# Kernel tuning notes

Measured on AMD Instinct MI355X. Metric: run time of the kernel, lower is better.

## Reference

```python
import jax, jax.numpy as jnp
import numpy as np

B_, T_, DIM, HID, OUT, TAG = 128, 256, 512, 1024, 512, 64

def hard_sigmoid(x):
    return jnp.clip(0.2 * x + 0.5, 0.0, 1.0)

def setup_inputs() -> dict:
    key = jax.random.key(0)
    ks = jax.random.split(key, 8)
    s = 0.02  # weight scale for numerical stability under softmax
    return {
        "x": jax.random.normal(ks[0], (B_, T_, DIM), jnp.float32),
        "x0": jnp.zeros((B_, OUT), jnp.float32),
        "s0": jnp.zeros((B_, HID), jnp.float32),
        "W": jax.random.normal(ks[1], (OUT, 3 * HID), jnp.float32) * s,
        "U": jax.random.normal(ks[2], (HID, 3 * HID), jnp.float32) * s,
        "b": jnp.zeros((3 * HID,), jnp.float32),
        "W_x": jax.random.normal(ks[3], (HID, OUT), jnp.float32) * s,
        "b_x": jnp.zeros((OUT,), jnp.float32),
        "V_r": jax.random.normal(ks[4], (DIM, HID), jnp.float32) * s,
        "V_z": jax.random.normal(ks[5], (DIM, HID), jnp.float32) * s,
        "V_s": jax.random.normal(ks[6], (DIM, HID), jnp.float32) * s,
        "W_y": jax.random.normal(ks[7], (OUT, TAG), jnp.float32) * s,
        "b_y": jnp.zeros((TAG,), jnp.float32),
    }

def reference(x, x0, s0, W, U, b, W_x, b_x, V_r, V_z, V_s, W_y, b_y):
    h = HID
    W_r, W_z, W_s = W[:, :h], W[:, h:2*h], W[:, 2*h:]
    U_r, U_z, U_s = U[:, :h], U[:, h:2*h], U[:, 2*h:]
    b_r, b_z, b_s = b[:h], b[h:2*h], b[2*h:]

    def step(carry, inp):
        x_tm1, s_tm1 = carry
        xr = x_tm1 @ W_r + b_r + inp @ V_r
        xz = x_tm1 @ W_z + b_z + inp @ V_z
        r = hard_sigmoid(xr + s_tm1 @ U_r)
        z = hard_sigmoid(xz + s_tm1 @ U_z)
        xs = x_tm1 @ W_s + b_s + inp @ V_s
        s1 = jnp.tanh(xs + (r * s_tm1) @ U_s)
        s_t = (1.0 - z) * s_tm1 + z * s1
        x_t = jax.nn.softmax(s_t @ W_x + b_x, axis=-1)
        t_t = jax.nn.softmax(x_t @ W_y + b_y, axis=-1)
        return (x_t, s_t), t_t

    xs_seq = jnp.swapaxes(x, 0, 1)  # [T, B, dim]
    (_, _), t_seq = jax.lax.scan(step, (x0, s0), xs_seq)
    return jnp.swapaxes(t_seq, 0, 1)  # [B, T, tag]
```

## Files before the change

kernel.cpp:

```cpp
#include <hip/hip_runtime.h>
#include <math.h>

#define B_    128
#define T_    256
#define DIM_  512
#define HID_  1024
#define OUT_  512
#define TAG_  64
#define K3_   3072

typedef float f32x4 __attribute__((ext_vector_type(4)));
typedef short bf16x8 __attribute__((ext_vector_type(8)));
typedef unsigned uint32x4 __attribute__((ext_vector_type(4)));

#define MFMA(a,b,c) __builtin_amdgcn_mfma_f32_16x16x32_bf16(a,b,c,0,0,0)
#define DRAINV do{ asm volatile("s_waitcnt vmcnt(0)" ::: "memory"); __builtin_amdgcn_sched_barrier(0); }while(0)

__device__ __forceinline__ unsigned short f2b(float f){
    unsigned int u = __float_as_uint(f);
    u = (u + 0x7fffu + ((u >> 16) & 1u)) >> 16;
    return (unsigned short)u;
}
__device__ __forceinline__ float hardsig(float x){
    return fminf(fmaxf(0.2f*x + 0.5f, 0.f), 1.f);
}
__device__ __forceinline__ uint32x4 ld16(const void* p){
    return *(const uint32x4*)p;
}
__device__ __forceinline__ uint32x4 pack8f(const float* p){
    float4 a = *(const float4*)p;
    float4 b = *(const float4*)(p + 4);
    uint32x4 r;
    r.x = ((unsigned)f2b(a.y) << 16) | f2b(a.x);
    r.y = ((unsigned)f2b(a.w) << 16) | f2b(a.z);
    r.z = ((unsigned)f2b(b.y) << 16) | f2b(b.x);
    r.w = ((unsigned)f2b(b.w) << 16) | f2b(b.z);
    return r;
}

__global__ __launch_bounds__(256) void k_tr(
    unsigned short* __restrict__ dst, int dstride,
    const float* __restrict__ src, int ld, int col_off)
{
    __shared__ float tile[32][33];
    const int kb = blockIdx.x * 32, nb = blockIdx.y * 32;
    const int tx = threadIdx.x & 31, ty = threadIdx.x >> 5;
    #pragma unroll
    for (int i = 0; i < 4; ++i){
        int kl = ty + i*8;
        tile[kl][tx] = src[(size_t)(kb + kl)*ld + col_off + nb + tx];
    }
    __syncthreads();
    #pragma unroll
    for (int i = 0; i < 4; ++i){
        int nl = ty + i*8;
        dst[(size_t)(nb + nl)*dstride + kb + tx] = f2b(tile[tx][nl]);
    }
}
__global__ __launch_bounds__(256) void k_cvtx(
    const float4* __restrict__ src, ushort4* __restrict__ dst, int n4)
{
    int i = blockIdx.x * 256 + threadIdx.x;
    if (i < n4){
        float4 v = src[i];
        ushort4 o;
        o.x = f2b(v.x); o.y = f2b(v.y); o.z = f2b(v.z); o.w = f2b(v.w);
        dst[i] = o;
    }
}
__global__ __launch_bounds__(256) void k_init(
    const float* __restrict__ x0, const float* __restrict__ s0,
    unsigned short* __restrict__ xbufB, float* __restrict__ s_f,
    unsigned short* __restrict__ s_b)
{
    int i = blockIdx.x * 256 + threadIdx.x;
    if (i < B_*OUT_) xbufB[i] = f2b(x0[i]);
    if (i < B_*HID_){ s_f[i] = s0[i]; s_b[i] = f2b(s0[i]); }
}

__global__ __launch_bounds__(512) void k_gA(
    const unsigned short* __restrict__ xb16, const float* __restrict__ xf, int use_xb,
    const unsigned short* __restrict__ Wcat, const float* __restrict__ bias,
    const unsigned short* __restrict__ xbufB, const unsigned short* __restrict__ s_bb,
    const float* __restrict__ spf,
    unsigned short* __restrict__ rs_bb, float* __restrict__ pre_z,
    float* __restrict__ pre_xs, int t)
{
    __shared__ __align__(16) char smem[131072];
    const int wg   = blockIdx.x;
    const int tid  = threadIdx.x;
    const int lane = tid & 63;
    const int wv   = tid >> 6;
    const int l15  = lane & 15;
    const int kch  = lane >> 4;
    const int mt   = wv >> 2;
    const int ns   = wv & 3;
    const int axor = l15 & 7;

    const int npA = wg % 24, mpA = wg / 24;
    const int m0A = mpA*32, cA = npA*128, nsegA = npA >> 3;

    if (nsegA < 2){
        #pragma unroll
        for (int j = 0; j < 16; ++j){
            const int c = tid + j*512, row = c >> 8, k16 = c & 255;
            const int gr = m0A + row;
            uint32x4 v;
            if (k16 < 64)       v = ld16(xbufB + gr*512 + k16*8);
            else if (k16 < 128){
                if (use_xb)     v = ld16(xb16 + ((size_t)gr*T_ + t)*DIM_ + (k16-64)*8);
                else            v = pack8f(xf + ((size_t)gr*T_ + t)*DIM_ + (k16-64)*8);
            } else              v = ld16(s_bb + gr*1024 + (k16-128)*8);
            *(uint32x4*)(smem + row*4096 + ((k16 ^ (row & 7)) << 4)) = v;
        }
    } else {
        #pragma unroll
        for (int j = 0; j < 8; ++j){
            const int c = tid + j*512, row = c >> 7, k16 = c & 127;
            const int gr = m0A + row;
            uint32x4 v;
            if (k16 < 64)       v = ld16(xbufB + gr*512 + k16*8);
            else {
                if (use_xb)     v = ld16(xb16 + ((size_t)gr*T_ + t)*DIM_ + (k16-64)*8);
                else            v = pack8f(xf + ((size_t)gr*T_ + t)*DIM_ + (k16-64)*8);
            }
            *(uint32x4*)(smem + row*4096 + ((k16 ^ (row & 7)) << 4)) = v;
        }
    }
    __syncthreads();

    const int c0 = cA + ns*32;
    const int kmax = (nsegA < 2) ? 2048 : 1024;
    const unsigned short* bp0 = Wcat + (size_t)(c0 + l15)*2048 + kch*8;
    const unsigned short* bp1 = bp0 + (size_t)16*2048;
    f32x4 acc0 = {0.f,0.f,0.f,0.f}, acc1 = {0.f,0.f,0.f,0.f};
    const int abase = (mt*16 + l15)*4096;
    #pragma unroll 8
    for (int kb = 0; kb < kmax; kb += 32){
        bf16x8 a = *(const bf16x8*)(smem + abase + ((((kb>>3)+kch) ^ axor) << 4));
        acc0 = MFMA(a, *(const bf16x8*)(bp0 + kb), acc0);
        acc1 = MFMA(a, *(const bf16x8*)(bp1 + kb), acc1);
    }
    const int rbA = m0A + mt*16 + kch*4;
    if (nsegA == 0){
        #pragma unroll
        for (int h = 0; h < 2; ++h){
            f32x4 acc = h ? acc1 : acc0;
            const int col = c0 + h*16 + l15;
            const float bv = bias[col];
            #pragma unroll
            for (int q = 0; q < 4; ++q){
                float rs = hardsig(acc[q] + bv) * spf[(size_t)(rbA+q)*1024 + col];
                rs_bb[(size_t)(rbA+q)*1024 + col] = f2b(rs);
            }
        }
    } else if (nsegA == 1){
        #pragma unroll
        for (int h = 0; h < 2; ++h){
            f32x4 acc = h ? acc1 : acc0;
            const int col = c0 + h*16 + l15;
            const float bv = bias[col];
            #pragma unroll
            for (int q = 0; q < 4; ++q)
                pre_z[(size_t)(rbA+q)*1024 + (col - 1024)] = acc[q] + bv;
        }
    } else {
        #pragma unroll
        for (int h = 0; h < 2; ++h){
            f32x4 acc = h ? acc1 : acc0;
            const int col = c0 + h*16 + l15;
            const float bv = bias[col];
            #pragma unroll
            for (int q = 0; q < 4; ++q)
                pre_xs[(size_t)(rbA+q)*1024 + (col - 2048)] = acc[q] + bv;
        }
    }
}

__global__ __launch_bounds__(512) void k_gB(
    const unsigned short* __restrict__ Ust,
    const unsigned short* __restrict__ rs_bb,
    const float* __restrict__ pre_z, const float* __restrict__ pre_xs,
    const float* __restrict__ spf,
    float* __restrict__ snf, unsigned short* __restrict__ s_bb)
{
    __shared__ __align__(16) char smem[65536];
    const int wg   = blockIdx.x;
    const int tid  = threadIdx.x;
    const int lane = tid & 63;
    const int wv   = tid >> 6;
    const int l15  = lane & 15;
    const int kch  = lane >> 4;
    const int mt   = wv >> 2;
    const int ns   = wv & 3;
    const int axor = l15 & 7;
    const int np = wg % 8, mp = wg / 8;
    const int m0B = mp*32, cB = np*128;

    #pragma unroll
    for (int j = 0; j < 8; ++j){
        const int c = tid + j*512, row = c >> 7, k16 = c & 127;
        uint32x4 v = ld16(rs_bb + (size_t)(m0B+row)*1024 + k16*8);
        *(uint32x4*)(smem + row*2048 + ((k16 ^ (row & 7)) << 4)) = v;
    }
    __syncthreads();

    const int c0 = cB + ns*32;
    const unsigned short* bp0 = Ust + (size_t)(c0 + l15)*1024 + kch*8;
    const unsigned short* bp1 = bp0 + (size_t)16*1024;
    f32x4 acc0 = {0.f,0.f,0.f,0.f}, acc1 = {0.f,0.f,0.f,0.f};
    const int abase = (mt*16 + l15)*2048;
    #pragma unroll 8
    for (int kb = 0; kb < 1024; kb += 32){
        bf16x8 a = *(const bf16x8*)(smem + abase + ((((kb>>3)+kch) ^ axor) << 4));
        acc0 = MFMA(a, *(const bf16x8*)(bp0 + kb), acc0);
        acc1 = MFMA(a, *(const bf16x8*)(bp1 + kb), acc1);
    }
    const int rbB = m0B + mt*16 + kch*4;
    #pragma unroll
    for (int h = 0; h < 2; ++h){
        f32x4 acc = h ? acc1 : acc0;
        const int col = c0 + h*16 + l15;
        #pragma unroll
        for (int q = 0; q < 4; ++q){
            const size_t idx = (size_t)(rbB+q)*1024 + col;
            float z  = hardsig(pre_z[idx]);
            float sv = (1.f - z)*spf[idx] + z*tanhf(pre_xs[idx] + acc[q]);
            snf[idx]  = sv;
            s_bb[idx] = f2b(sv);
        }
    }
}

__global__ __launch_bounds__(512) void k_gC(
    const unsigned short* __restrict__ Wxt,
    const unsigned short* __restrict__ s_bb,
    const float* __restrict__ bx, float* __restrict__ logits)
{
    __shared__ __align__(16) char smem[65536];
    const int wg   = blockIdx.x;
    const int tid  = threadIdx.x;
    const int lane = tid & 63;
    const int wv   = tid >> 6;
    const int l15  = lane & 15;
    const int kch  = lane >> 4;
    const int mt   = wv >> 2;
    const int ns   = wv & 3;
    const int axor = l15 & 7;
    const int np = wg % 4, mp = wg / 4;
    const int m0C = mp*32, cC = np*128;

    #pragma unroll
    for (int j = 0; j < 8; ++j){
        const int c = tid + j*512, row = c >> 7, k16 = c & 127;
        uint32x4 v = ld16(s_bb + (size_t)(m0C+row)*1024 + k16*8);
        *(uint32x4*)(smem + row*2048 + ((k16 ^ (row & 7)) << 4)) = v;
    }
    __syncthreads();

    const int c0 = cC + ns*32;
    const unsigned short* bp0 = Wxt + (size_t)(c0 + l15)*1024 + kch*8;
    const unsigned short* bp1 = bp0 + (size_t)16*1024;
    f32x4 acc0 = {0.f,0.f,0.f,0.f}, acc1 = {0.f,0.f,0.f,0.f};
    const int abase = (mt*16 + l15)*2048;
    #pragma unroll 8
    for (int kb = 0; kb < 1024; kb += 32){
        bf16x8 a = *(const bf16x8*)(smem + abase + ((((kb>>3)+kch) ^ axor) << 4));
        acc0 = MFMA(a, *(const bf16x8*)(bp0 + kb), acc0);
        acc1 = MFMA(a, *(const bf16x8*)(bp1 + kb), acc1);
    }
    const int rbC = m0C + mt*16 + kch*4;
    #pragma unroll
    for (int h = 0; h < 2; ++h){
        f32x4 acc = h ? acc1 : acc0;
        const int col = c0 + h*16 + l15;
        const float bv = bx[col];
        #pragma unroll
        for (int q = 0; q < 4; ++q)
            logits[(size_t)(rbC+q)*512 + col] = acc[q] + bv;
    }
}

__global__ __launch_bounds__(256) void k_soft(
    const float* __restrict__ logits, const float* __restrict__ Wy,
    const float* __restrict__ by, unsigned short* __restrict__ xbufB,
    float* __restrict__ out, int t)
{
    __shared__ float xs[512];
    __shared__ float red[256];
    const int r = blockIdx.x, tid = threadIdx.x;
    float v0 = logits[r*OUT_ + tid];
    float v1 = logits[r*OUT_ + 256 + tid];
    red[tid] = fmaxf(v0, v1);
    __syncthreads();
    for (int s = 128; s > 0; s >>= 1){
        if (tid < s) red[tid] = fmaxf(red[tid], red[tid+s]);
        __syncthreads();
    }
    float mx = red[0];
    __syncthreads();
    float e0 = expf(v0 - mx), e1 = expf(v1 - mx);
    red[tid] = e0 + e1;
    __syncthreads();
    for (int s = 128; s > 0; s >>= 1){
        if (tid < s) red[tid] += red[tid+s];
        __syncthreads();
    }
    float inv = 1.f / red[0];
    __syncthreads();
    float x0v = e0*inv, x1v = e1*inv;
    xs[tid] = x0v; xs[tid + 256] = x1v;
    xbufB[r*OUT_ + tid] = f2b(x0v);
    xbufB[r*OUT_ + 256 + tid] = f2b(x1v);
    __syncthreads();
    const int j = tid & 63, part = tid >> 6;
    float p = 0.f;
    const int k0 = part * 128;
    #pragma unroll 4
    for (int k = k0; k < k0 + 128; ++k) p += xs[k] * Wy[k*TAG_ + j];
    red[tid] = p;
    __syncthreads();
    if (tid < 64){
        float tl = red[tid] + red[tid+64] + red[tid+128] + red[tid+192] + by[tid];
        float wm = tl;
        #pragma unroll
        for (int off = 32; off > 0; off >>= 1) wm = fmaxf(wm, __shfl_xor(wm, off));
        float ex = expf(tl - wm);
        float sm = ex;
        #pragma unroll
        for (int off = 32; off > 0; off >>= 1) sm += __shfl_xor(sm, off);
        out[((long)r*T_ + t)*TAG_ + tid] = ex / sm;
    }
}

extern "C" void kernel_launch(void* const* d_in, const int* in_sizes, int n_in,
                              void* d_out, int out_size, void* d_ws, size_t ws_size,
                              hipStream_t stream){
    const float* x   = (const float*)d_in[0];
    const float* x0  = (const float*)d_in[1];
    const float* s0  = (const float*)d_in[2];
    const float* W   = (const float*)d_in[3];
    const float* U   = (const float*)d_in[4];
    const float* b   = (const float*)d_in[5];
    const float* Wx  = (const float*)d_in[6];
    const float* bx  = (const float*)d_in[7];
    const float* Vr  = (const float*)d_in[8];
    const float* Vz  = (const float*)d_in[9];
    const float* Vs  = (const float*)d_in[10];
    const float* Wy  = (const float*)d_in[11];
    const float* by  = (const float*)d_in[12];
    float* out = (float*)d_out;

    char* ws = (char*)d_ws;
    size_t off = 0;
    auto alloc = [&](size_t bytes) -> size_t {
        size_t o = off; off = (off + bytes + 255) & ~(size_t)255; return o;
    };
    unsigned short* Wcat = (unsigned short*)(ws + alloc((size_t)K3_*2048*2));
    unsigned short* Ust  = (unsigned short*)(ws + alloc((size_t)HID_*HID_*2));
    unsigned short* Wxt  = (unsigned short*)(ws + alloc((size_t)OUT_*HID_*2));
    unsigned short* xbufB= (unsigned short*)(ws + alloc((size_t)B_*OUT_*2));
    unsigned short* s_b  = (unsigned short*)(ws + alloc((size_t)B_*HID_*2));
    unsigned short* rs_b = (unsigned short*)(ws + alloc((size_t)B_*HID_*2));
    float* s_f    = (float*)(ws + alloc((size_t)2*B_*HID_*4));
    float* pre_z  = (float*)(ws + alloc((size_t)B_*HID_*4));
    float* pre_xs = (float*)(ws + alloc((size_t)B_*HID_*4));
    float* logits = (float*)(ws + alloc((size_t)B_*OUT_*4));
    unsigned short* xb16 = (unsigned short*)(ws + alloc((size_t)B_*T_*DIM_*2));
    int use_xb = (off <= ws_size) ? 1 : 0;

    k_tr<<<dim3(16, 96), 256, 0, stream>>>(Wcat,                           2048, W,  K3_,  0);
    k_tr<<<dim3(16, 32), 256, 0, stream>>>(Wcat + 512,                     2048, Vr, HID_, 0);
    k_tr<<<dim3(16, 32), 256, 0, stream>>>(Wcat + (size_t)1024*2048 + 512, 2048, Vz, HID_, 0);
    k_tr<<<dim3(16, 32), 256, 0, stream>>>(Wcat + (size_t)2048*2048 + 512, 2048, Vs, HID_, 0);
    k_tr<<<dim3(32, 64), 256, 0, stream>>>(Wcat + 1024,                    2048, U,  K3_,  0);
    k_tr<<<dim3(32, 32), 256, 0, stream>>>(Ust,                            1024, U,  K3_,  2048);
    k_tr<<<dim3(32, 16), 256, 0, stream>>>(Wxt,                            1024, Wx, OUT_, 0);
    if (use_xb){
        int n4 = B_*T_*DIM_/4;
        k_cvtx<<<(n4 + 255)/256, 256, 0, stream>>>((const float4*)x, (ushort4*)xb16, n4);
    }
    k_init<<<(B_*HID_ + 255)/256, 256, 0, stream>>>(x0, s0, xbufB, s_f, s_b);

    for (int t = 0; t < T_; ++t){
        float* spf = s_f + (size_t)(t & 1)*(B_*HID_);
        float* snf = s_f + (size_t)((t & 1)^1)*(B_*HID_);
        k_gA  <<< 96, 512, 0, stream>>>(xb16, x, use_xb, Wcat, b, xbufB, s_b, spf,
                                        rs_b, pre_z, pre_xs, t);
        k_gB  <<< 32, 512, 0, stream>>>(Ust, rs_b, pre_z, pre_xs, spf, snf, s_b);
        k_gC  <<< 16, 512, 0, stream>>>(Wxt, s_b, bx, logits);
        k_soft<<<128, 256, 0, stream>>>(logits, Wy, by, xbufB, out, t);
    }
}
```

Before: 19.73 ms.

## Fuse output GEMM with both softmaxes into one per-row-block kernel

Merges the W_x GEMM kernel and the softmax/W_y/softmax kernel into a single kernel where each of 8 workgroups owns 16 batch rows and all 512 output columns. Logits stay in shared memory, which removes one launch per timestep and the global logits round trip. The cost is far less parallelism: only 8 workgroups now run the GEMM, and each reads all of W_x, so per-block latency and the serial W_y loop per thread (512 iterations) grow.

```diff
diff --git a/kernel.cpp b/kernel.cpp
--- a/kernel.cpp
+++ b/kernel.cpp
@@ -14,7 +14,6 @@
 typedef unsigned uint32x4 __attribute__((ext_vector_type(4)));
 
 #define MFMA(a,b,c) __builtin_amdgcn_mfma_f32_16x16x32_bf16(a,b,c,0,0,0)
-#define DRAINV do{ asm volatile("s_waitcnt vmcnt(0)" ::: "memory"); __builtin_amdgcn_sched_barrier(0); }while(0)
 
 __device__ __forceinline__ unsigned short f2b(float f){
     unsigned int u = __float_as_uint(f);
@@ -232,105 +231,99 @@
     }
 }
 
-__global__ __launch_bounds__(512) void k_gC(
+__global__ __launch_bounds__(512) void k_gCD(
     const unsigned short* __restrict__ Wxt,
     const unsigned short* __restrict__ s_bb,
-    const float* __restrict__ bx, float* __restrict__ logits)
-{
-    __shared__ __align__(16) char smem[65536];
-    const int wg   = blockIdx.x;
+    const float* __restrict__ bx,
+    const float* __restrict__ Wy,
+    const float* __restrict__ by,
+    unsigned short* __restrict__ xbufB,
+    float* __restrict__ out, int t)
+{
+    __shared__ __align__(16) char smem[32768];
+    __shared__ float lg[16][516];
+    const int g    = blockIdx.x;
     const int tid  = threadIdx.x;
     const int lane = tid & 63;
     const int wv   = tid >> 6;
     const int l15  = lane & 15;
     const int kch  = lane >> 4;
-    const int mt   = wv >> 2;
-    const int ns   = wv & 3;
-    const int axor = l15 & 7;
-    const int np = wg % 4, mp = wg / 4;
-    const int m0C = mp*32, cC = np*128;
-
-    #pragma unroll
-    for (int j = 0; j < 8; ++j){
+
+    #pragma unroll
+    for (int j = 0; j < 4; ++j){
         const int c = tid + j*512, row = c >> 7, k16 = c & 127;
-        uint32x4 v = ld16(s_bb + (size_t)(m0C+row)*1024 + k16*8);
+        uint32x4 v = ld16(s_bb + (size_t)(g*16 + row)*1024 + k16*8);
         *(uint32x4*)(smem + row*2048 + ((k16 ^ (row & 7)) << 4)) = v;
     }
     __syncthreads();
 
-    const int c0 = cC + ns*32;
+    const int c0 = wv*64;
     const unsigned short* bp0 = Wxt + (size_t)(c0 + l15)*1024 + kch*8;
     const unsigned short* bp1 = bp0 + (size_t)16*1024;
-    f32x4 acc0 = {0.f,0.f,0.f,0.f}, acc1 = {0.f,0.f,0.f,0.f};
-    const int abase = (mt*16 + l15)*2048;
+    const unsigned short* bp2 = bp0 + (size_t)32*1024;
+    const unsigned short* bp3 = bp0 + (size_t)48*1024;
+    f32x4 a0={0.f,0.f,0.f,0.f}, a1={0.f,0.f,0.f,0.f};
+    f32x4 a2={0.f,0.f,0.f,0.f}, a3={0.f,0.f,0.f,0.f};
+    const int abase = l15*2048;
+    const int axor  = l15 & 7;
     #pragma unroll 8
     for (int kb = 0; kb < 1024; kb += 32){
         bf16x8 a = *(const bf16x8*)(smem + abase + ((((kb>>3)+kch) ^ axor) << 4));
-        acc0 = MFMA(a, *(const bf16x8*)(bp0 + kb), acc0);
-        acc1 = MFMA(a, *(const bf16x8*)(bp1 + kb), acc1);
-    }
-    const int rbC = m0C + mt*16 + kch*4;
-    #pragma unroll
-    for (int h = 0; h < 2; ++h){
-        f32x4 acc = h ? acc1 : acc0;
-        const int col = c0 + h*16 + l15;
-        const float bv = bx[col];
-        #pragma unroll
-        for (int q = 0; q < 4; ++q)
-            logits[(size_t)(rbC+q)*512 + col] = acc[q] + bv;
-    }
-}
-
-__global__ __launch_bounds__(256) void k_soft(
-    const float* __restrict__ logits, const float* __restrict__ Wy,
-    const float* __restrict__ by, unsigned short* __restrict__ xbufB,
-    float* __restrict__ out, int t)
-{
-    __shared__ float xs[512];
-    __shared__ float red[256];
-    const int r = blockIdx.x, tid = threadIdx.x;
-    float v0 = logits[r*OUT_ + tid];
-    float v1 = logits[r*OUT_ + 256 + tid];
-    red[tid] = fmaxf(v0, v1);
-    __syncthreads();
-    for (int s = 128; s > 0; s >>= 1){
-        if (tid < s) red[tid] = fmaxf(red[tid], red[tid+s]);
-        __syncthreads();
-    }
-    float mx = red[0];
-    __syncthreads();
-    float e0 = expf(v0 - mx), e1 = expf(v1 - mx);
-    red[tid] = e0 + e1;
-    __syncthreads();
-    for (int s = 128; s > 0; s >>= 1){
-        if (tid < s) red[tid] += red[tid+s];
-        __syncthreads();
-    }
-    float inv = 1.f / red[0];
-    __syncthreads();
-    float x0v = e0*inv, x1v = e1*inv;
-    xs[tid] = x0v; xs[tid + 256] = x1v;
-    xbufB[r*OUT_ + tid] = f2b(x0v);
-    xbufB[r*OUT_ + 256 + tid] = f2b(x1v);
-    __syncthreads();
-    const int j = tid & 63, part = tid >> 6;
-    float p = 0.f;
-    const int k0 = part * 128;
+        a0 = MFMA(a, *(const bf16x8*)(bp0 + kb), a0);
+        a1 = MFMA(a, *(const bf16x8*)(bp1 + kb), a1);
+        a2 = MFMA(a, *(const bf16x8*)(bp2 + kb), a2);
+        a3 = MFMA(a, *(const bf16x8*)(bp3 + kb), a3);
+    }
+    #pragma unroll
+    for (int q = 0; q < 4; ++q){
+        const int row = kch*4 + q;
+        lg[row][c0      + l15] = a0[q] + bx[c0      + l15];
+        lg[row][c0 + 16 + l15] = a1[q] + bx[c0 + 16 + l15];
+        lg[row][c0 + 32 + l15] = a2[q] + bx[c0 + 32 + l15];
+        lg[row][c0 + 48 + l15] = a3[q] + bx[c0 + 48 + l15];
+    }
+    __syncthreads();
+
+    const int row = tid >> 5, l32 = tid & 31;
+    const int gr  = g*16 + row;
+    float v[16];
+    float mx = -3.0e38f;
+    #pragma unroll
+    for (int i = 0; i < 16; ++i){ v[i] = lg[row][l32 + i*32]; mx = fmaxf(mx, v[i]); }
+    #pragma unroll
+    for (int off = 16; off > 0; off >>= 1) mx = fmaxf(mx, __shfl_xor(mx, off));
+    float s = 0.f;
+    #pragma unroll
+    for (int i = 0; i < 16; ++i){ v[i] = expf(v[i] - mx); s += v[i]; }
+    #pragma unroll
+    for (int off = 16; off > 0; off >>= 1) s += __shfl_xor(s, off);
+    const float inv = 1.f / s;
+    #pragma unroll
+    for (int i = 0; i < 16; ++i){
+        float xv = v[i] * inv;
+        lg[row][l32 + i*32] = xv;
+        xbufB[gr*512 + l32 + i*32] = f2b(xv);
+    }
+    __syncthreads();
+
+    float p0 = 0.f, p1 = 0.f;
     #pragma unroll 4
-    for (int k = k0; k < k0 + 128; ++k) p += xs[k] * Wy[k*TAG_ + j];
-    red[tid] = p;
-    __syncthreads();
-    if (tid < 64){
-        float tl = red[tid] + red[tid+64] + red[tid+128] + red[tid+192] + by[tid];
-        float wm = tl;
-        #pragma unroll
-        for (int off = 32; off > 0; off >>= 1) wm = fmaxf(wm, __shfl_xor(wm, off));
-        float ex = expf(tl - wm);
-        float sm = ex;
-        #pragma unroll
-        for (int off = 32; off > 0; off >>= 1) sm += __shfl_xor(sm, off);
-        out[((long)r*T_ + t)*TAG_ + tid] = ex / sm;
-    }
+    for (int k = 0; k < 512; ++k){
+        float xv = lg[row][k];
+        p0 += xv * Wy[k*TAG_ + l32];
+        p1 += xv * Wy[k*TAG_ + l32 + 32];
+    }
+    p0 += by[l32]; p1 += by[l32 + 32];
+    float m2 = fmaxf(p0, p1);
+    #pragma unroll
+    for (int off = 16; off > 0; off >>= 1) m2 = fmaxf(m2, __shfl_xor(m2, off));
+    float e0 = expf(p0 - m2), e1 = expf(p1 - m2);
+    float s2 = e0 + e1;
+    #pragma unroll
+    for (int off = 16; off > 0; off >>= 1) s2 += __shfl_xor(s2, off);
+    const float inv2 = 1.f / s2;
+    out[((size_t)gr*T_ + t)*TAG_ + l32]      = e0 * inv2;
+    out[((size_t)gr*T_ + t)*TAG_ + l32 + 32] = e1 * inv2;
 }
 
 extern "C" void kernel_launch(void* const* d_in, const int* in_sizes, int n_in,
@@ -365,7 +358,6 @@
     float* s_f    = (float*)(ws + alloc((size_t)2*B_*HID_*4));
     float* pre_z  = (float*)(ws + alloc((size_t)B_*HID_*4));
     float* pre_xs = (float*)(ws + alloc((size_t)B_*HID_*4));
-    float* logits = (float*)(ws + alloc((size_t)B_*OUT_*4));
     unsigned short* xb16 = (unsigned short*)(ws + alloc((size_t)B_*T_*DIM_*2));
     int use_xb = (off <= ws_size) ? 1 : 0;
 
@@ -385,10 +377,9 @@
     for (int t = 0; t < T_; ++t){
         float* spf = s_f + (size_t)(t & 1)*(B_*HID_);
         float* snf = s_f + (size_t)((t & 1)^1)*(B_*HID_);
-        k_gA  <<< 96, 512, 0, stream>>>(xb16, x, use_xb, Wcat, b, xbufB, s_b, spf,
-                                        rs_b, pre_z, pre_xs, t);
-        k_gB  <<< 32, 512, 0, stream>>>(Ust, rs_b, pre_z, pre_xs, spf, snf, s_b);
-        k_gC  <<< 16, 512, 0, stream>>>(Wxt, s_b, bx, logits);
-        k_soft<<<128, 256, 0, stream>>>(logits, Wy, by, xbufB, out, t);
-    }
-}
+        k_gA <<<96, 512, 0, stream>>>(xb16, x, use_xb, Wcat, b, xbufB, s_b, spf,
+                                      rs_b, pre_z, pre_xs, t);
+        k_gB <<<32, 512, 0, stream>>>(Ust, rs_b, pre_z, pre_xs, spf, snf, s_b);
+        k_gCD<<< 8, 512, 0, stream>>>(Wxt, s_b, bx, Wy, by, xbufB, out, t);
+    }
+}
```

After: 25.66 ms. 1.3x slower.
